# Performance work log

Measured on AMD Instinct MI355X. Metric: run time of the kernel, lower is better.

## Reference

```python
import jax, jax.numpy as jnp
import numpy as np

N = 100000
E = 1600000
IN_CH = 128
HID = 32
HEADS = 8
OUT_CH = 40
NEG_SLOPE = 0.2


def _glorot(key, shape):
    fan = shape[0] + shape[-1]
    return jax.random.normal(key, shape, dtype=jnp.float32) * jnp.sqrt(2.0 / fan)


def gat_conv(x, src, dst, W, att_src, att_dst, bias, heads, out_ch, concat):
    # PyG GATConv (eval mode, dropout inactive, self-loops already appended)
    n = x.shape[0]
    h = (x @ W).reshape(n, heads, out_ch)              # [N,H,C]
    a_s = jnp.sum(h * att_src, axis=-1)                # [N,H]
    a_d = jnp.sum(h * att_dst, axis=-1)                # [N,H]
    e = jax.nn.leaky_relu(a_s[src] + a_d[dst], NEG_SLOPE)  # [E,H]
    # softmax over incoming edges of each destination node
    m = jax.ops.segment_max(e, dst, num_segments=n)
    e = jnp.exp(e - m[dst])
    denom = jax.ops.segment_sum(e, dst, num_segments=n)
    alpha = e / denom[dst]                              # [E,H]
    msg = h[src] * alpha[:, :, None]                    # [E,H,C] gather + weight
    out = jax.ops.segment_sum(msg, dst, num_segments=n)  # [N,H,C] scatter-add
    if concat:
        out = out.reshape(n, heads * out_ch)
    else:
        out = out.mean(axis=1)
    return out + bias


def setup_inputs() -> dict:
    key = jax.random.key(0)
    ks = jax.random.split(key, 16)
    x = jax.random.normal(ks[0], (N, IN_CH), dtype=jnp.float32)
    edge_index = jax.random.randint(ks[1], (2, E), 0, N, dtype=jnp.int64)
    params = {
        "W1": _glorot(ks[2], (IN_CH, HEADS * HID)),
        "as1": _glorot(ks[3], (HEADS, HID)),
        "ad1": _glorot(ks[4], (HEADS, HID)),
        "b1": jnp.zeros((HEADS * HID,), jnp.float32),
        "W2": _glorot(ks[5], (HEADS * HID, HID)),
        "as2": _glorot(ks[6], (1, HID)),
        "ad2": _glorot(ks[7], (1, HID)),
        "b2": jnp.zeros((HID,), jnp.float32),
        "W3": _glorot(ks[8], (HID, OUT_CH)),
        "as3": _glorot(ks[9], (1, OUT_CH)),
        "ad3": _glorot(ks[10], (1, OUT_CH)),
        "b3": jnp.zeros((OUT_CH,), jnp.float32),
    }
    return {"x": x, "edge_index": edge_index, **params}


def reference(x, edge_index, W1, as1, ad1, b1, W2, as2, ad2, b2, W3, as3, ad3, b3):
    n = x.shape[0]
    # PyG GATConv adds self-loops by default
    loops = jnp.arange(n, dtype=edge_index.dtype)
    src = jnp.concatenate([edge_index[0], loops])
    dst = jnp.concatenate([edge_index[1], loops])

    h = gat_conv(x, src, dst, W1, as1, ad1, b1, HEADS, HID, concat=True)
    h = jax.nn.elu(h)
    h = gat_conv(h, src, dst, W2, as2, ad2, b2, 1, HID, concat=False)
    h = jax.nn.elu(h)
    h = gat_conv(h, src, dst, W3, as3, ad3, b3, 1, OUT_CH, concat=False)
    return jax.nn.log_softmax(h, axis=1)
```

## Files before the change

### kernel.cpp

```cpp
#include <hip/hip_runtime.h>

#define NN 100000
#define NE 1600000
#define ET 1700000
#define NEG 0.2f
#define FNEG 3.4e38f
#define NBSC 98
#define GEMM1_NB 1563
#define PE_NB 6641
#define FATA_NB 8305
#define FILL_CH 425000

#define SRC_OFF   0ULL
#define DST_OFF   6800000ULL
#define RP_OFF    13600000ULL
#define CSR_OFF   14400128ULL
#define W1F_OFF   21200128ULL
#define W2F_OFF   21265664ULL
#define W3F_OFF   21282048ULL
#define SC_OFF    21285120ULL
#define H_OFF     21286144ULL
#define H2B_OFF   72486144ULL
#define H3B_OFF   88486144ULL
#define AS3_OFF   123686144ULL
#define AD3_OFF   124086144ULL
#define ASN_OFF   150886144ULL
#define ADN_OFF   154086144ULL
#define AS2_OFF   157286144ULL
#define AD2_OFF   157686144ULL
#define CNT_OFF   158086144ULL
#define RANK_OFF  164486144ULL
#define WS_NEED   171286144ULL

typedef short bf16x8 __attribute__((ext_vector_type(8)));
typedef float f32x4 __attribute__((ext_vector_type(4)));
typedef float f32x2 __attribute__((ext_vector_type(2)));

__device__ __forceinline__ float lrelu(float x) { return x > 0.f ? x : NEG * x; }
__device__ __forceinline__ float b2f(unsigned short u) {
  return __uint_as_float(((unsigned)u) << 16);
}
__device__ __forceinline__ unsigned short f2bu(float f) {
  unsigned u = __float_as_uint(f);
  return (unsigned short)((u + 0x7FFFu + ((u >> 16) & 1u)) >> 16);
}

__global__ __launch_bounds__(256) void k_sentinel(float* out, int n) {
  int i = blockIdx.x * 256 + threadIdx.x;
  if (i < n) out[i] = 12345.0f;
}

__global__ __launch_bounds__(256) void k_prep_w(const float* __restrict__ W1,
                                                const float* __restrict__ W2,
                                                const float* __restrict__ W3,
                                                unsigned short* __restrict__ W1f,
                                                unsigned short* __restrict__ W2f,
                                                unsigned short* __restrict__ W3f) {
  int idx = blockIdx.x * 256 + threadIdx.x;
  if (idx < 4096) {
    int fg = idx >> 6, lane = idx & 63;
    int mf = fg >> 2, kk = fg & 3;
    int c = mf * 16 + (lane & 15), k0 = kk * 32 + (lane >> 4) * 8;
    unsigned short* o = W1f + idx * 8;
    #pragma unroll
    for (int j = 0; j < 8; ++j) o[j] = f2bu(W1[(k0 + j) * 256 + c]);
  } else if (idx < 5120) {
    int t = idx - 4096;
    int fg = t >> 6, lane = t & 63;
    int mf = fg >> 3, kk = fg & 7;
    int c = mf * 16 + (lane & 15), k0 = kk * 32 + (lane >> 4) * 8;
    unsigned short* o = W2f + t * 8;
    #pragma unroll
    for (int j = 0; j < 8; ++j) o[j] = f2bu(W2[(k0 + j) * 32 + c]);
  } else if (idx < 5312) {
    int t = idx - 5120;
    int mf = t >> 6, lane = t & 63;
    int c = mf * 16 + (lane & 15), k0 = (lane >> 4) * 8;
    unsigned short* o = W3f + t * 8;
    #pragma unroll
    for (int j = 0; j < 8; ++j) o[j] = (c < 40) ? f2bu(W3[(k0 + j) * 40 + c]) : 0;
  }
}

__global__ __launch_bounds__(256) void k_fatA(const int* __restrict__ raw,
                                              int* __restrict__ src,
                                              int* __restrict__ dst,
                                              int* __restrict__ cnt,
                                              int* __restrict__ rank,
                                              const float* __restrict__ x,
                                              const bf16x8* __restrict__ W1f,
                                              const float* __restrict__ as1,
                                              const float* __restrict__ ad1,
                                              unsigned char* __restrict__ h8,
                                              float* __restrict__ a_s,
                                              float* __restrict__ a_d) {
  __shared__ __align__(16) unsigned short xs[64 * 128];
  __shared__ float asL[256], adL[256];
  const int bid = blockIdx.x;
  const int grp = bid / 5, rem = bid - grp * 5;
  const int tid = threadIdx.x;

  if (rem != 4) {
    int pe = grp * 4 + rem;
    if (pe >= PE_NB) return;
    bool is64 = true;
    #pragma unroll
    for (int i = 1; i < 32; i += 2) is64 = is64 && (raw[i] == 0);
    long long e = (long long)pe * 256 + tid;
    if (e >= ET) return;
    int s, d;
    if (e < NE) {
      if (is64) {
        const long long* r = (const long long*)raw;
        s = (int)r[e];
        d = (int)r[NE + e];
      } else {
        s = raw[e];
        d = raw[NE + e];
      }
    } else {
      s = d = (int)(e - NE);
    }
    src[e] = s;
    dst[e] = d;
    rank[e] = atomicAdd(&cnt[d * 16 + (tid & 7)], 1);
    return;
  }

  if (grp >= GEMM1_NB) return;
  const int n0 = grp * 64;
  asL[tid] = as1[tid];
  adL[tid] = ad1[tid];
  for (int j = tid; j < 2048; j += 256) {
    int r = j >> 5;
    int c4 = (j & 31) << 2;
    long long row = n0 + r; if (row >= NN) row = NN - 1;
    float4 v = *(const float4*)(x + row * 128 + c4);
    unsigned short* p = &xs[r * 128 + c4];
    p[0] = f2bu(v.x); p[1] = f2bu(v.y); p[2] = f2bu(v.z); p[3] = f2bu(v.w);
  }
  __syncthreads();
  const int w = tid >> 6, lane = tid & 63;
  const int nloc = w * 16 + (lane & 15);
  const int node = n0 + nloc;
  bf16x8 bfr[4];
  #pragma unroll
  for (int kk = 0; kk < 4; ++kk)
    bfr[kk] = *(const bf16x8*)&xs[nloc * 128 + kk * 32 + (lane >> 4) * 8];
  const int ch_base = (lane >> 4) * 4;
  float sA[8] = {}, sD[8] = {};
  #pragma unroll
  for (int mf = 0; mf < 16; ++mf) {
    f32x4 acc = {0.f, 0.f, 0.f, 0.f};
    #pragma unroll
    for (int kk = 0; kk < 4; ++kk) {
      bf16x8 af = W1f[(mf * 4 + kk) * 64 + lane];
      acc = __builtin_amdgcn_mfma_f32_16x16x32_bf16(af, bfr[kk], acc, 0, 0, 0);
    }
    const float* av = &asL[mf * 16 + ch_base];
    const float* dv = &adL[mf * 16 + ch_base];
    float ps = acc[0] * av[0] + acc[1] * av[1] + acc[2] * av[2] + acc[3] * av[3];
    float pd = acc[0] * dv[0] + acc[1] * dv[1] + acc[2] * dv[2] + acc[3] * dv[3];
    ps += __shfl_xor(ps, 16); ps += __shfl_xor(ps, 32);
    pd += __shfl_xor(pd, 16); pd += __shfl_xor(pd, 32);
    sA[mf >> 1] += ps; sD[mf >> 1] += pd;
    if (node < NN) {
      int w01 = __builtin_amdgcn_cvt_pk_fp8_f32(acc[0], acc[1], 0, false);
      int w0123 = __builtin_amdgcn_cvt_pk_fp8_f32(acc[2], acc[3], w01, true);
      *(unsigned*)&h8[(unsigned)(node * 256 + mf * 16 + ch_base)] = (unsigned)w0123;
    }
  }
  if (lane < 16 && node < NN) {
    #pragma unroll
    for (int hd = 0; hd < 8; ++hd) {
      a_s[node * 8 + hd] = sA[hd];
      a_d[node * 8 + hd] = sD[hd];
    }
  }
}

__global__ __launch_bounds__(1024) void k_scan_a(int* __restrict__ cnt,
                                                 int* __restrict__ rowptr,
                                                 int* __restrict__ bsum) {
  __shared__ int wsum[16];
  const int lane = threadIdx.x & 63, wid = threadIdx.x >> 6;
  int i = blockIdx.x * 1024 + threadIdx.x;
  int x = 0;
  if (i < NN) {
    int run = 0;
    #pragma unroll
    for (int k = 0; k < 8; ++k) {
      int c = cnt[i * 16 + k];
      cnt[i * 16 + k] = run;
      run += c;
    }
    x = run;
  }
  int inc = x;
  #pragma unroll
  for (int off = 1; off < 64; off <<= 1) {
    int t = __shfl_up(inc, off);
    if (lane >= off) inc += t;
  }
  if (lane == 63) wsum[wid] = inc;
  __syncthreads();
  if (wid == 0) {
    int w = (lane < 16) ? wsum[lane] : 0;
    #pragma unroll
    for (int off = 1; off < 16; off <<= 1) {
      int t = __shfl_up(w, off);
      if (lane >= off) w += t;
    }
    if (lane < 16) wsum[lane] = w;
  }
  __syncthreads();
  int base = wid ? wsum[wid - 1] : 0;
  if (i < NN) rowptr[i + 1] = base + inc;
  if (threadIdx.x == 1023) bsum[blockIdx.x] = base + inc;
}

__global__ __launch_bounds__(128) void k_scan_b(int* __restrict__ bsum) {
  __shared__ int w0tot;
  int tid = threadIdx.x;
  int v = (tid < NBSC) ? bsum[tid] : 0;
  int inc = v;
  #pragma unroll
  for (int off = 1; off < 64; off <<= 1) {
    int t = __shfl_up(inc, off);
    if ((tid & 63) >= off) inc += t;
  }
  if (tid == 63) w0tot = inc;
  __syncthreads();
  if (tid >= 64) inc += w0tot;
  if (tid < NBSC) bsum[tid] = inc - v;
}

__global__ __launch_bounds__(1024) void k_scan_c(int* __restrict__ rowptr,
                                                 const int* __restrict__ bsum) {
  int i = blockIdx.x * 1024 + threadIdx.x;
  if (i < NN) rowptr[i + 1] += bsum[blockIdx.x];
  if (i == 0) rowptr[0] = 0;
}

__global__ __launch_bounds__(256) void k_fill_nr(const int* __restrict__ src,
                                                 const int* __restrict__ dst,
                                                 const int* __restrict__ rank,
                                                 const int* __restrict__ cnt,
                                                 const int* __restrict__ rowptr,
                                                 int* __restrict__ csr) {
  int gid = blockIdx.x * 256 + threadIdx.x;
  if (gid >= FILL_CH) return;
  const int h = gid & 7;
  int e0 = gid, e1 = gid + FILL_CH, e2 = gid + 2 * FILL_CH, e3 = gid + 3 * FILL_CH;
  int d0 = dst[e0], d1 = dst[e1], d2 = dst[e2], d3 = dst[e3];
  int r0 = rank[e0], r1 = rank[e1], r2 = rank[e2], r3 = rank[e3];
  int s0 = src[e0], s1 = src[e1], s2 = src[e2], s3 = src[e3];
  int p0 = cnt[d0 * 16 + h], p1 = cnt[d1 * 16 + h];
  int p2 = cnt[d2 * 16 + h], p3 = cnt[d3 * 16 + h];
  int b0 = rowptr[d0], b1 = rowptr[d1], b2 = rowptr[d2], b3 = rowptr[d3];
  csr[b0 + p0 + r0] = s0;
  csr[b1 + p1 + r1] = s1;
  csr[b2 + p2 + r2] = s2;
  csr[b3 + p3 + r3] = s3;
}

__global__ __launch_bounds__(1024) void k_gather1f(const int* __restrict__ rowptr,
                                                   const int* __restrict__ csr,
                                                   const float* __restrict__ as1n,
                                                   const float* __restrict__ ad1n,
                                                   const unsigned char* __restrict__ h8,
                                                   const float* __restrict__ b,
                                                   const bf16x8* __restrict__ W2f,
                                                   const float* __restrict__ as2,
                                                   const float* __restrict__ ad2,
                                                   unsigned short* __restrict__ h2,
                                                   float* __restrict__ a_s2o,
                                                   float* __restrict__ a_d2o) {
  __shared__ __align__(16) unsigned short xs[16 * 256];
  const int tid = threadIdx.x;
  const int w = tid >> 6, lane = tid & 63;
  const int n0 = blockIdx.x * 16;
  const int node = n0 + w;
  const int beg = __builtin_amdgcn_readfirstlane(rowptr[node]);
  const int end = __builtin_amdgcn_readfirstlane(rowptr[node + 1]);

  {
  }
  const int hd = lane & 7;
  const int eg = lane >> 3;
  const float adv1 = ad1n[node * 8 + hd];
  float mx = -FNEG, sm = 0.f;
  for (int i = beg + eg; i < end; i += 8) {
    float v = lrelu(as1n[csr[i] * 8 + hd] + adv1);
    float nm = fmaxf(mx, v);
    sm = sm * __expf(mx - nm) + __expf(v - nm);
    mx = nm;
  }
  #pragma unroll
  for (int off = 8; off < 64; off <<= 1) {
    float mo = __shfl_xor(mx, off);
    float so = __shfl_xor(sm, off);
    float nm = fmaxf(mx, mo);
    sm = sm * __expf(mx - nm) + so * __expf(mo - nm);
    mx = nm;
  }
  const int hd2 = lane >> 3;
  const float m2 = __shfl(mx, hd2);
  const float rden = 1.0f / __shfl(sm, hd2);
  const float adv2 = ad1n[node * 8 + hd2];

  const unsigned l4 = lane * 4;
  float4 acc = {0.f, 0.f, 0.f, 0.f};
  int i = beg;
  for (; i + 8 <= end; i += 8) {
    int s0 = __builtin_amdgcn_readfirstlane(csr[i]);
    int s1 = __builtin_amdgcn_readfirstlane(csr[i + 1]);
    int s2 = __builtin_amdgcn_readfirstlane(csr[i + 2]);
    int s3 = __builtin_amdgcn_readfirstlane(csr[i + 3]);
    int s4 = __builtin_amdgcn_readfirstlane(csr[i + 4]);
    int s5 = __builtin_amdgcn_readfirstlane(csr[i + 5]);
    int s6 = __builtin_amdgcn_readfirstlane(csr[i + 6]);
    int s7 = __builtin_amdgcn_readfirstlane(csr[i + 7]);
    float u0 = as1n[(unsigned)(s0 * 8) + hd2];
    float u1 = as1n[(unsigned)(s1 * 8) + hd2];
    float u2 = as1n[(unsigned)(s2 * 8) + hd2];
    float u3 = as1n[(unsigned)(s3 * 8) + hd2];
    float u4 = as1n[(unsigned)(s4 * 8) + hd2];
    float u5 = as1n[(unsigned)(s5 * 8) + hd2];
    float u6 = as1n[(unsigned)(s6 * 8) + hd2];
    float u7 = as1n[(unsigned)(s7 * 8) + hd2];
    unsigned w0 = *(const unsigned*)(h8 + ((unsigned)(s0 << 8) + l4));
    unsigned w1 = *(const unsigned*)(h8 + ((unsigned)(s1 << 8) + l4));
    unsigned w2 = *(const unsigned*)(h8 + ((unsigned)(s2 << 8) + l4));
    unsigned w3 = *(const unsigned*)(h8 + ((unsigned)(s3 << 8) + l4));
    unsigned w4 = *(const unsigned*)(h8 + ((unsigned)(s4 << 8) + l4));
    unsigned w5 = *(const unsigned*)(h8 + ((unsigned)(s5 << 8) + l4));
    unsigned w6 = *(const unsigned*)(h8 + ((unsigned)(s6 << 8) + l4));
    unsigned w7 = *(const unsigned*)(h8 + ((unsigned)(s7 << 8) + l4));
    float a0 = __expf(lrelu(u0 + adv2) - m2) * rden;
    float a1 = __expf(lrelu(u1 + adv2) - m2) * rden;
    float a2 = __expf(lrelu(u2 + adv2) - m2) * rden;
    float a3 = __expf(lrelu(u3 + adv2) - m2) * rden;
    float a4 = __expf(lrelu(u4 + adv2) - m2) * rden;
    float a5 = __expf(lrelu(u5 + adv2) - m2) * rden;
    float a6 = __expf(lrelu(u6 + adv2) - m2) * rden;
    float a7 = __expf(lrelu(u7 + adv2) - m2) * rden;
    f32x2 lo, hi;
    lo = __builtin_amdgcn_cvt_pk_f32_fp8(w0, false); hi = __builtin_amdgcn_cvt_pk_f32_fp8(w0, true);
    acc.x += a0 * lo[0]; acc.y += a0 * lo[1]; acc.z += a0 * hi[0]; acc.w += a0 * hi[1];
    lo = __builtin_amdgcn_cvt_pk_f32_fp8(w1, false); hi = __builtin_amdgcn_cvt_pk_f32_fp8(w1, true);
    acc.x += a1 * lo[0]; acc.y += a1 * lo[1]; acc.z += a1 * hi[0]; acc.w += a1 * hi[1];
    lo = __builtin_amdgcn_cvt_pk_f32_fp8(w2, false); hi = __builtin_amdgcn_cvt_pk_f32_fp8(w2, true);
    acc.x += a2 * lo[0]; acc.y += a2 * lo[1]; acc.z += a2 * hi[0]; acc.w += a2 * hi[1];
    lo = __builtin_amdgcn_cvt_pk_f32_fp8(w3, false); hi = __builtin_amdgcn_cvt_pk_f32_fp8(w3, true);
    acc.x += a3 * lo[0]; acc.y += a3 * lo[1]; acc.z += a3 * hi[0]; acc.w += a3 * hi[1];
    lo = __builtin_amdgcn_cvt_pk_f32_fp8(w4, false); hi = __builtin_amdgcn_cvt_pk_f32_fp8(w4, true);
    acc.x += a4 * lo[0]; acc.y += a4 * lo[1]; acc.z += a4 * hi[0]; acc.w += a4 * hi[1];
    lo = __builtin_amdgcn_cvt_pk_f32_fp8(w5, false); hi = __builtin_amdgcn_cvt_pk_f32_fp8(w5, true);
    acc.x += a5 * lo[0]; acc.y += a5 * lo[1]; acc.z += a5 * hi[0]; acc.w += a5 * hi[1];
    lo = __builtin_amdgcn_cvt_pk_f32_fp8(w6, false); hi = __builtin_amdgcn_cvt_pk_f32_fp8(w6, true);
    acc.x += a6 * lo[0]; acc.y += a6 * lo[1]; acc.z += a6 * hi[0]; acc.w += a6 * hi[1];
    lo = __builtin_amdgcn_cvt_pk_f32_fp8(w7, false); hi = __builtin_amdgcn_cvt_pk_f32_fp8(w7, true);
    acc.x += a7 * lo[0]; acc.y += a7 * lo[1]; acc.z += a7 * hi[0]; acc.w += a7 * hi[1];
  }
  for (; i < end; ++i) {
    int s0 = __builtin_amdgcn_readfirstlane(csr[i]);
    float u0 = as1n[(unsigned)(s0 * 8) + hd2];
    unsigned w0 = *(const unsigned*)(h8 + ((unsigned)(s0 << 8) + l4));
    float a0 = __expf(lrelu(u0 + adv2) - m2) * rden;
    f32x2 lo = __builtin_amdgcn_cvt_pk_f32_fp8(w0, false);
    f32x2 hi = __builtin_amdgcn_cvt_pk_f32_fp8(w0, true);
    acc.x += a0 * lo[0]; acc.y += a0 * lo[1]; acc.z += a0 * hi[0]; acc.w += a0 * hi[1];
  }
  float4 bv = *(const float4*)(b + l4);
  acc.x += bv.x; acc.y += bv.y; acc.z += bv.z; acc.w += bv.w;
  acc.x = acc.x > 0.f ? acc.x : expm1f(acc.x);
  acc.y = acc.y > 0.f ? acc.y : expm1f(acc.y);
  acc.z = acc.z > 0.f ? acc.z : expm1f(acc.z);
  acc.w = acc.w > 0.f ? acc.w : expm1f(acc.w);
  {
    ushort4 o;
    o.x = f2bu(acc.x); o.y = f2bu(acc.y); o.z = f2bu(acc.z); o.w = f2bu(acc.w);
    *(ushort4*)&xs[w * 256 + l4] = o;
  }
  __syncthreads();
  if (w == 0) {
    const int nloc = lane & 15;
    const int node2 = n0 + nloc;
    const int ch_base = (lane >> 4) * 4;
    float sA = 0.f, sD = 0.f;
    #pragma unroll
    for (int mf = 0; mf < 2; ++mf) {
      f32x4 c2 = {0.f, 0.f, 0.f, 0.f};
      #pragma unroll
      for (int kk = 0; kk < 8; ++kk) {
        bf16x8 bfr = *(const bf16x8*)&xs[nloc * 256 + kk * 32 + (lane >> 4) * 8];
        c2 = __builtin_amdgcn_mfma_f32_16x16x32_bf16(W2f[(mf * 8 + kk) * 64 + lane],
                                                     bfr, c2, 0, 0, 0);
      }
      float4 av = *(const float4*)(as2 + mf * 16 + ch_base);
      float4 dv = *(const float4*)(ad2 + mf * 16 + ch_base);
      float ps = c2[0] * av.x + c2[1] * av.y + c2[2] * av.z + c2[3] * av.w;
      float pd = c2[0] * dv.x + c2[1] * dv.y + c2[2] * dv.z + c2[3] * dv.w;
      ps += __shfl_xor(ps, 16); ps += __shfl_xor(ps, 32);
      pd += __shfl_xor(pd, 16); pd += __shfl_xor(pd, 32);
      sA += ps; sD += pd;
      ushort4 o;
      o.x = f2bu(c2[0]); o.y = f2bu(c2[1]); o.z = f2bu(c2[2]); o.w = f2bu(c2[3]);
      *(ushort4*)&h2[(unsigned)(node2 * 32 + mf * 16 + ch_base)] = o;
    }
    if (lane < 16) { a_s2o[node2] = sA; a_d2o[node2] = sD; }
  }
}

__global__ __launch_bounds__(512) void k_gather2f(const int* __restrict__ rowptr,
                                                  const int* __restrict__ csr,
                                                  const float* __restrict__ a_s,
                                                  const float* __restrict__ a_d,
                                                  const unsigned short* __restrict__ h,
                                                  const float* __restrict__ b,
                                                  const bf16x8* __restrict__ W3f,
                                                  const float* __restrict__ as3,
                                                  const float* __restrict__ ad3,
                                                  unsigned short* __restrict__ h3,
                                                  float* __restrict__ a_s3o,
                                                  float* __restrict__ a_d3o) {
  __shared__ __align__(16) unsigned short xs[16 * 32];
  const int tid = threadIdx.x;
  const int hw = tid >> 5, lane32 = tid & 31;
  const int n0 = blockIdx.x * 16;
  const int node = n0 + hw;
  const int beg = rowptr[node], end = rowptr[node + 1];
  const float adv = a_d[node];

  float mx = -FNEG, sm = 0.f;
  for (int i = beg + lane32; i < end; i += 32) {
    float v = lrelu(a_s[csr[i]] + adv);
    float nm = fmaxf(mx, v);
    sm = sm * __expf(mx - nm) + __expf(v - nm);
    mx = nm;
  }
  #pragma unroll
  for (int off = 1; off < 32; off <<= 1) {
    float mo = __shfl_xor(mx, off, 32);
    float so = __shfl_xor(sm, off, 32);
    float nm = fmaxf(mx, mo);
    sm = sm * __expf(mx - nm) + so * __expf(mo - nm);
    mx = nm;
  }
  float rden = 1.0f / sm;

  float acc = 0.f;
  int i = beg;
  for (; i + 4 <= end; i += 4) {
    int s0 = csr[i], s1 = csr[i + 1], s2 = csr[i + 2], s3 = csr[i + 3];
    float a0 = __expf(lrelu(a_s[s0] + adv) - mx) * rden;
    float a1 = __expf(lrelu(a_s[s1] + adv) - mx) * rden;
    float a2 = __expf(lrelu(a_s[s2] + adv) - mx) * rden;
    float a3 = __expf(lrelu(a_s[s3] + adv) - mx) * rden;
    unsigned short v0 = h[(unsigned)(s0 * 32 + lane32)];
    unsigned short v1 = h[(unsigned)(s1 * 32 + lane32)];
    unsigned short v2 = h[(unsigned)(s2 * 32 + lane32)];
    unsigned short v3 = h[(unsigned)(s3 * 32 + lane32)];
    acc += a0 * b2f(v0) + a1 * b2f(v1) + a2 * b2f(v2) + a3 * b2f(v3);
  }
  for (; i < end; ++i) {
    int s0 = csr[i];
    float a0 = __expf(lrelu(a_s[s0] + adv) - mx) * rden;
    acc += a0 * b2f(h[(unsigned)(s0 * 32 + lane32)]);
  }
  acc += b[lane32];
  acc = acc > 0.f ? acc : expm1f(acc);
  xs[hw * 32 + lane32] = f2bu(acc);
  __syncthreads();
  if (tid < 64) {
    const int lane = tid;
    const int nloc = lane & 15;
    const int node3 = n0 + nloc;
    const int ch_base = (lane >> 4) * 4;
    bf16x8 bfr = *(const bf16x8*)&xs[nloc * 32 + (lane >> 4) * 8];
    float sA = 0.f, sD = 0.f;
    #pragma unroll
    for (int mf = 0; mf < 3; ++mf) {
      f32x4 c3 = {0.f, 0.f, 0.f, 0.f};
      c3 = __builtin_amdgcn_mfma_f32_16x16x32_bf16(W3f[mf * 64 + lane], bfr, c3, 0, 0, 0);
      int ch0 = mf * 16 + ch_base;
      float4 av = {0.f, 0.f, 0.f, 0.f}, dv = {0.f, 0.f, 0.f, 0.f};
      if (ch0 < 40) {
        av = *(const float4*)(as3 + ch0);
        dv = *(const float4*)(ad3 + ch0);
      }
      float ps = c3[0] * av.x + c3[1] * av.y + c3[2] * av.z + c3[3] * av.w;
      float pd = c3[0] * dv.x + c3[1] * dv.y + c3[2] * dv.z + c3[3] * dv.w;
      ps += __shfl_xor(ps, 16); ps += __shfl_xor(ps, 32);
      pd += __shfl_xor(pd, 16); pd += __shfl_xor(pd, 32);
      sA += ps; sD += pd;
      if (ch0 < 40) {
        ushort4 o;
        o.x = f2bu(c3[0]); o.y = f2bu(c3[1]); o.z = f2bu(c3[2]); o.w = f2bu(c3[3]);
        *(ushort4*)&h3[(unsigned)(node3 * 40 + ch0)] = o;
      }
    }
    if (lane < 16) { a_s3o[node3] = sA; a_d3o[node3] = sD; }
  }
}

__global__ __launch_bounds__(256) void k_gather3f(const int* __restrict__ rowptr,
                                                  const int* __restrict__ csr,
                                                  const float* __restrict__ a_s,
                                                  const float* __restrict__ a_d,
                                                  const unsigned short* __restrict__ h,
                                                  const float* __restrict__ b,
                                                  float* __restrict__ out) {
  const int node = blockIdx.x * 4 + (threadIdx.x >> 6);
  const int lane = threadIdx.x & 63;
  const int beg = __builtin_amdgcn_readfirstlane(rowptr[node]);
  const int end = __builtin_amdgcn_readfirstlane(rowptr[node + 1]);
  const float adv = a_d[node];

  float mx = -FNEG, sm = 0.f;
  for (int i = beg + lane; i < end; i += 64) {
    float v = lrelu(a_s[csr[i]] + adv);
    float nm = fmaxf(mx, v);
    sm = sm * __expf(mx - nm) + __expf(v - nm);
    mx = nm;
  }
  #pragma unroll
  for (int off = 1; off < 64; off <<= 1) {
    float mo = __shfl_xor(mx, off);
    float so = __shfl_xor(sm, off);
    float nm = fmaxf(mx, mo);
    sm = sm * __expf(mx - nm) + so * __expf(mo - nm);
    mx = nm;
  }
  float rden = 1.0f / sm;

  float acc = 0.f;
  int i = beg;
  for (; i + 4 <= end; i += 4) {
    int s0 = __builtin_amdgcn_readfirstlane(csr[i]);
    int s1 = __builtin_amdgcn_readfirstlane(csr[i + 1]);
    int s2 = __builtin_amdgcn_readfirstlane(csr[i + 2]);
    int s3 = __builtin_amdgcn_readfirstlane(csr[i + 3]);
    float a0 = __expf(lrelu(a_s[s0] + adv) - mx) * rden;
    float a1 = __expf(lrelu(a_s[s1] + adv) - mx) * rden;
    float a2 = __expf(lrelu(a_s[s2] + adv) - mx) * rden;
    float a3 = __expf(lrelu(a_s[s3] + adv) - mx) * rden;
    if (lane < 40) {
      unsigned short v0 = h[(unsigned)(s0 * 40 + lane)];
      unsigned short v1 = h[(unsigned)(s1 * 40 + lane)];
      unsigned short v2 = h[(unsigned)(s2 * 40 + lane)];
      unsigned short v3 = h[(unsigned)(s3 * 40 + lane)];
      acc += a0 * b2f(v0) + a1 * b2f(v1) + a2 * b2f(v2) + a3 * b2f(v3);
    }
  }
  for (; i < end; ++i) {
    int s0 = __builtin_amdgcn_readfirstlane(csr[i]);
    float a0 = __expf(lrelu(a_s[s0] + adv) - mx) * rden;
    if (lane < 40) acc += a0 * b2f(h[(unsigned)(s0 * 40 + lane)]);
  }
  float v = (lane < 40) ? acc + b[lane] : -FNEG;
  float vmax = v;
  #pragma unroll
  for (int off = 1; off < 64; off <<= 1) vmax = fmaxf(vmax, __shfl_xor(vmax, off));
  float ex = (lane < 40) ? __expf(v - vmax) : 0.f;
  float es = ex;
  #pragma unroll
  for (int off = 1; off < 64; off <<= 1) es += __shfl_xor(es, off);
  float lse = vmax + __logf(es);
  if (lane < 40) out[(long long)node * 40 + lane] = v - lse;
}

extern "C" void kernel_launch(void* const* d_in, const int* in_sizes, int n_in,
                              void* d_out, int out_size, void* d_ws, size_t ws_size,
                              hipStream_t stream) {
  const float* x   = (const float*)d_in[0];
  const int*   eix = (const int*)d_in[1];
  const float* W1  = (const float*)d_in[2];
  const float* as1 = (const float*)d_in[3];
  const float* ad1 = (const float*)d_in[4];
  const float* b1  = (const float*)d_in[5];
  const float* W2  = (const float*)d_in[6];
  const float* as2 = (const float*)d_in[7];
  const float* ad2 = (const float*)d_in[8];
  const float* b2  = (const float*)d_in[9];
  const float* W3  = (const float*)d_in[10];
  const float* as3 = (const float*)d_in[11];
  const float* ad3 = (const float*)d_in[12];
  const float* b3  = (const float*)d_in[13];
  float* out = (float*)d_out;

  if (ws_size < WS_NEED) {
    k_sentinel<<<(out_size + 255) / 256, 256, 0, stream>>>(out, out_size);
    return;
  }

  char* ws = (char*)d_ws;
  int*    src    = (int*)(ws + SRC_OFF);
  int*    dst    = (int*)(ws + DST_OFF);
  int*    rowptr = (int*)(ws + RP_OFF);
  int*    csr    = (int*)(ws + CSR_OFF);
  unsigned short* W1f = (unsigned short*)(ws + W1F_OFF);
  unsigned short* W2f = (unsigned short*)(ws + W2F_OFF);
  unsigned short* W3f = (unsigned short*)(ws + W3F_OFF);
  int*    bsum   = (int*)(ws + SC_OFF);
  unsigned char*  h1q  = (unsigned char*)(ws + H_OFF);
  unsigned short* h2b  = (unsigned short*)(ws + H2B_OFF);
  unsigned short* h3b  = (unsigned short*)(ws + H3B_OFF);
  float*  aS1    = (float*)(ws + ASN_OFF);
  float*  aD1    = (float*)(ws + ADN_OFF);
  float*  aS2    = (float*)(ws + AS2_OFF);
  float*  aD2    = (float*)(ws + AD2_OFF);
  float*  aS3    = (float*)(ws + AS3_OFF);
  float*  aD3    = (float*)(ws + AD3_OFF);
  int*    cnt    = (int*)(ws + CNT_OFF);
  int*    rank   = (int*)(ws + RANK_OFF);

  hipMemsetAsync(ws + CNT_OFF, 0, 6400000, stream);
  k_prep_w<<<21, 256, 0, stream>>>(W1, W2, W3, W1f, W2f, W3f);
  k_fatA<<<FATA_NB, 256, 0, stream>>>(eix, src, dst, cnt, rank, x,
                                      (const bf16x8*)W1f, as1, ad1, h1q, aS1, aD1);
  k_scan_a<<<NBSC, 1024, 0, stream>>>(cnt, rowptr, bsum);
  k_scan_b<<<1, 128, 0, stream>>>(bsum);
  k_scan_c<<<NBSC, 1024, 0, stream>>>(rowptr, bsum);
  k_fill_nr<<<(FILL_CH + 255) / 256, 256, 0, stream>>>(src, dst, rank, cnt,
                                                       rowptr, csr);

  k_gather1f<<<NN / 16, 1024, 0, stream>>>(rowptr, csr, aS1, aD1, h1q, b1,
                                           (const bf16x8*)W2f, as2, ad2,
                                           h2b, aS2, aD2);

  k_gather2f<<<NN / 16, 512, 0, stream>>>(rowptr, csr, aS2, aD2, h2b, b2,
                                          (const bf16x8*)W3f, as3, ad3,
                                          h3b, aS3, aD3);

  k_gather3f<<<NN / 4, 256, 0, stream>>>(rowptr, csr, aS3, aD3, h3b, b3, out);
}
```

Before: 400.0 us.

## Transpose degree counters to sub-bucket-major and cache layer-1 attention weights in LDS

The per-destination 8-way atomic counters move from a padded node-major layout (16 ints per node) to a dense sub-bucket-major layout, which halves the memset and makes the scan reads coalesced. In the layer-1 gather, the softmax attention coefficients for up to 64 incoming edges per node are computed once per (edge, head) into shared memory after the max/sum pass. The aggregation loop then reads them from LDS instead of re-gathering as1n and recomputing exp per lane. This adds 32KB of LDS per block, which may lower occupancy, and nodes with more than 64 edges fall back to the old path.

```diff
diff --git a/kernel.cpp b/kernel.cpp
--- a/kernel.cpp
+++ b/kernel.cpp
@@ -10,6 +10,7 @@
 #define PE_NB 6641
 #define FATA_NB 8305
 #define FILL_CH 425000
+#define DCAP 64
 
 #define SRC_OFF   0ULL
 #define DST_OFF   6800000ULL
@@ -85,7 +86,7 @@
 __global__ __launch_bounds__(256) void k_fatA(const int* __restrict__ raw,
                                               int* __restrict__ src,
                                               int* __restrict__ dst,
-                                              int* __restrict__ cnt,
+                                              int* __restrict__ cnt8,
                                               int* __restrict__ rank,
                                               const float* __restrict__ x,
                                               const bf16x8* __restrict__ W1f,
@@ -123,7 +124,7 @@
     }
     src[e] = s;
     dst[e] = d;
-    rank[e] = atomicAdd(&cnt[d * 16 + (tid & 7)], 1);
+    rank[e] = atomicAdd(&cnt8[(tid & 7) * NN + d], 1);
     return;
   }
 
@@ -179,7 +180,7 @@
   }
 }
 
-__global__ __launch_bounds__(1024) void k_scan_a(int* __restrict__ cnt,
+__global__ __launch_bounds__(1024) void k_scan_a(int* __restrict__ cnt8,
                                                  int* __restrict__ rowptr,
                                                  int* __restrict__ bsum) {
   __shared__ int wsum[16];
@@ -190,8 +191,8 @@
     int run = 0;
     #pragma unroll
     for (int k = 0; k < 8; ++k) {
-      int c = cnt[i * 16 + k];
-      cnt[i * 16 + k] = run;
+      int c = cnt8[k * NN + i];
+      cnt8[k * NN + i] = run;
       run += c;
     }
     x = run;
@@ -245,7 +246,7 @@
 __global__ __launch_bounds__(256) void k_fill_nr(const int* __restrict__ src,
                                                  const int* __restrict__ dst,
                                                  const int* __restrict__ rank,
-                                                 const int* __restrict__ cnt,
+                                                 const int* __restrict__ cnt8,
                                                  const int* __restrict__ rowptr,
                                                  int* __restrict__ csr) {
   int gid = blockIdx.x * 256 + threadIdx.x;
@@ -255,8 +256,8 @@
   int d0 = dst[e0], d1 = dst[e1], d2 = dst[e2], d3 = dst[e3];
   int r0 = rank[e0], r1 = rank[e1], r2 = rank[e2], r3 = rank[e3];
   int s0 = src[e0], s1 = src[e1], s2 = src[e2], s3 = src[e3];
-  int p0 = cnt[d0 * 16 + h], p1 = cnt[d1 * 16 + h];
-  int p2 = cnt[d2 * 16 + h], p3 = cnt[d3 * 16 + h];
+  int p0 = cnt8[h * NN + d0], p1 = cnt8[h * NN + d1];
+  int p2 = cnt8[h * NN + d2], p3 = cnt8[h * NN + d3];
   int b0 = rowptr[d0], b1 = rowptr[d1], b2 = rowptr[d2], b3 = rowptr[d3];
   csr[b0 + p0 + r0] = s0;
   csr[b1 + p1 + r1] = s1;
@@ -277,6 +278,7 @@
                                                    float* __restrict__ a_s2o,
                                                    float* __restrict__ a_d2o) {
   __shared__ __align__(16) unsigned short xs[16 * 256];
+  __shared__ float alds[16 * DCAP * 8];
   const int tid = threadIdx.x;
   const int w = tid >> 6, lane = tid & 63;
   const int n0 = blockIdx.x * 16;
@@ -284,8 +286,6 @@
   const int beg = __builtin_amdgcn_readfirstlane(rowptr[node]);
   const int end = __builtin_amdgcn_readfirstlane(rowptr[node + 1]);
 
-  {
-  }
   const int hd = lane & 7;
   const int eg = lane >> 3;
   const float adv1 = ad1n[node * 8 + hd];
@@ -304,15 +304,24 @@
     sm = sm * __expf(mx - nm) + so * __expf(mo - nm);
     mx = nm;
   }
+  const float rdenh = 1.0f / sm;
+
+  float* al = &alds[w * (DCAP * 8)];
+  const int dcap = (end - beg <= DCAP) ? end : beg + DCAP;
+  for (int i = beg + eg; i < dcap; i += 8) {
+    float v = lrelu(as1n[csr[i] * 8 + hd] + adv1);
+    al[(i - beg) * 8 + hd] = __expf(v - mx) * rdenh;
+  }
+
   const int hd2 = lane >> 3;
   const float m2 = __shfl(mx, hd2);
-  const float rden = 1.0f / __shfl(sm, hd2);
+  const float rden2 = __shfl(rdenh, hd2);
   const float adv2 = ad1n[node * 8 + hd2];
 
   const unsigned l4 = lane * 4;
   float4 acc = {0.f, 0.f, 0.f, 0.f};
   int i = beg;
-  for (; i + 8 <= end; i += 8) {
+  for (; i + 8 <= dcap; i += 8) {
     int s0 = __builtin_amdgcn_readfirstlane(csr[i]);
     int s1 = __builtin_amdgcn_readfirstlane(csr[i + 1]);
     int s2 = __builtin_amdgcn_readfirstlane(csr[i + 2]);
@@ -321,14 +330,6 @@
     int s5 = __builtin_amdgcn_readfirstlane(csr[i + 5]);
     int s6 = __builtin_amdgcn_readfirstlane(csr[i + 6]);
     int s7 = __builtin_amdgcn_readfirstlane(csr[i + 7]);
-    float u0 = as1n[(unsigned)(s0 * 8) + hd2];
-    float u1 = as1n[(unsigned)(s1 * 8) + hd2];
-    float u2 = as1n[(unsigned)(s2 * 8) + hd2];
-    float u3 = as1n[(unsigned)(s3 * 8) + hd2];
-    float u4 = as1n[(unsigned)(s4 * 8) + hd2];
-    float u5 = as1n[(unsigned)(s5 * 8) + hd2];
-    float u6 = as1n[(unsigned)(s6 * 8) + hd2];
-    float u7 = as1n[(unsigned)(s7 * 8) + hd2];
     unsigned w0 = *(const unsigned*)(h8 + ((unsigned)(s0 << 8) + l4));
     unsigned w1 = *(const unsigned*)(h8 + ((unsigned)(s1 << 8) + l4));
     unsigned w2 = *(const unsigned*)(h8 + ((unsigned)(s2 << 8) + l4));
@@ -337,14 +338,9 @@
     unsigned w5 = *(const unsigned*)(h8 + ((unsigned)(s5 << 8) + l4));
     unsigned w6 = *(const unsigned*)(h8 + ((unsigned)(s6 << 8) + l4));
     unsigned w7 = *(const unsigned*)(h8 + ((unsigned)(s7 << 8) + l4));
-    float a0 = __expf(lrelu(u0 + adv2) - m2) * rden;
-    float a1 = __expf(lrelu(u1 + adv2) - m2) * rden;
-    float a2 = __expf(lrelu(u2 + adv2) - m2) * rden;
-    float a3 = __expf(lrelu(u3 + adv2) - m2) * rden;
-    float a4 = __expf(lrelu(u4 + adv2) - m2) * rden;
-    float a5 = __expf(lrelu(u5 + adv2) - m2) * rden;
-    float a6 = __expf(lrelu(u6 + adv2) - m2) * rden;
-    float a7 = __expf(lrelu(u7 + adv2) - m2) * rden;
+    int o0 = (i - beg) * 8 + hd2;
+    float a0 = al[o0 +  0], a1 = al[o0 +  8], a2 = al[o0 + 16], a3 = al[o0 + 24];
+    float a4 = al[o0 + 32], a5 = al[o0 + 40], a6 = al[o0 + 48], a7 = al[o0 + 56];
     f32x2 lo, hi;
     lo = __builtin_amdgcn_cvt_pk_f32_fp8(w0, false); hi = __builtin_amdgcn_cvt_pk_f32_fp8(w0, true);
     acc.x += a0 * lo[0]; acc.y += a0 * lo[1]; acc.z += a0 * hi[0]; acc.w += a0 * hi[1];
@@ -363,11 +359,19 @@
     lo = __builtin_amdgcn_cvt_pk_f32_fp8(w7, false); hi = __builtin_amdgcn_cvt_pk_f32_fp8(w7, true);
     acc.x += a7 * lo[0]; acc.y += a7 * lo[1]; acc.z += a7 * hi[0]; acc.w += a7 * hi[1];
   }
+  for (; i < dcap; ++i) {
+    int s0 = __builtin_amdgcn_readfirstlane(csr[i]);
+    unsigned w0 = *(const unsigned*)(h8 + ((unsigned)(s0 << 8) + l4));
+    float a0 = al[(i - beg) * 8 + hd2];
+    f32x2 lo = __builtin_amdgcn_cvt_pk_f32_fp8(w0, false);
+    f32x2 hi = __builtin_amdgcn_cvt_pk_f32_fp8(w0, true);
+    acc.x += a0 * lo[0]; acc.y += a0 * lo[1]; acc.z += a0 * hi[0]; acc.w += a0 * hi[1];
+  }
   for (; i < end; ++i) {
     int s0 = __builtin_amdgcn_readfirstlane(csr[i]);
     float u0 = as1n[(unsigned)(s0 * 8) + hd2];
     unsigned w0 = *(const unsigned*)(h8 + ((unsigned)(s0 << 8) + l4));
-    float a0 = __expf(lrelu(u0 + adv2) - m2) * rden;
+    float a0 = __expf(lrelu(u0 + adv2) - m2) * rden2;
     f32x2 lo = __builtin_amdgcn_cvt_pk_f32_fp8(w0, false);
     f32x2 hi = __builtin_amdgcn_cvt_pk_f32_fp8(w0, true);
     acc.x += a0 * lo[0]; acc.y += a0 * lo[1]; acc.z += a0 * hi[0]; acc.w += a0 * hi[1];
@@ -613,17 +617,17 @@
   float*  aD2    = (float*)(ws + AD2_OFF);
   float*  aS3    = (float*)(ws + AS3_OFF);
   float*  aD3    = (float*)(ws + AD3_OFF);
-  int*    cnt    = (int*)(ws + CNT_OFF);
+  int*    cnt8   = (int*)(ws + CNT_OFF);
   int*    rank   = (int*)(ws + RANK_OFF);
 
-  hipMemsetAsync(ws + CNT_OFF, 0, 6400000, stream);
+  hipMemsetAsync(ws + CNT_OFF, 0, 3200000, stream);
   k_prep_w<<<21, 256, 0, stream>>>(W1, W2, W3, W1f, W2f, W3f);
-  k_fatA<<<FATA_NB, 256, 0, stream>>>(eix, src, dst, cnt, rank, x,
+  k_fatA<<<FATA_NB, 256, 0, stream>>>(eix, src, dst, cnt8, rank, x,
                                       (const bf16x8*)W1f, as1, ad1, h1q, aS1, aD1);
-  k_scan_a<<<NBSC, 1024, 0, stream>>>(cnt, rowptr, bsum);
+  k_scan_a<<<NBSC, 1024, 0, stream>>>(cnt8, rowptr, bsum);
   k_scan_b<<<1, 128, 0, stream>>>(bsum);
   k_scan_c<<<NBSC, 1024, 0, stream>>>(rowptr, bsum);
-  k_fill_nr<<<(FILL_CH + 255) / 256, 256, 0, stream>>>(src, dst, rank, cnt,
+  k_fill_nr<<<(FILL_CH + 255) / 256, 256, 0, stream>>>(src, dst, rank, cnt8,
                                                        rowptr, csr);
 
   k_gather1f<<<NN / 16, 1024, 0, stream>>>(rowptr, csr, aS1, aD1, h1q, b1,
```

Result: slower. 467.6 us (+16.9%).
